# Performance work log

Hardware: AMD Instinct MI355X
Metric: run time of the kernel (lower is better)

Reference implementation:

```python
import jax, jax.numpy as jnp
import numpy as np
from jax import lax

N, L, D = 8, 2048, 512
KS = [3, 5]
DECAY = 0.2


def setup_inputs() -> dict:
    key = jax.random.key(0)
    k1, k2, k3, k4, k5 = jax.random.split(key, 5)
    return {
        "qa_embed_data": jax.random.normal(k1, (N, L, D), dtype=jnp.float32),
        "conv_w3": jax.random.normal(k2, (D, 1, KS[0]), dtype=jnp.float32) * (1.0 / KS[0]),
        "conv_w5": jax.random.normal(k3, (D, 1, KS[1]), dtype=jnp.float32) * (1.0 / KS[1]),
        "fusion_w": jax.random.normal(k4, (D, 2 * D), dtype=jnp.float32) * 0.02,
        "fusion_b": jax.random.normal(k5, (D,), dtype=jnp.float32) * 0.02,
    }


def causal_depthwise_conv(x, w, k):
    # x: [N, L, C], w: [C, 1, k] (depthwise, groups=C). Left-pad by k-1 (causal).
    xc = jnp.transpose(x, (0, 2, 1))  # [N, C, L]
    y = lax.conv_general_dilated(
        xc, w, window_strides=(1,), padding=[(k - 1, 0)],
        feature_group_count=x.shape[-1],
        dimension_numbers=("NCH", "OIH", "NCH"))
    return jnp.transpose(y, (0, 2, 1))  # [N, L, C]


def squash(v):
    norm = jnp.linalg.norm(v, axis=-1, keepdims=True)
    scale = norm ** 2 / (1.0 + norm ** 2)
    return scale * v / (norm + 1e-9)


def dynamic_routing(u, num_iterations):
    # u: [N, L, M, C]
    n, l, m, _ = u.shape
    logits = jnp.zeros((n, l, m), dtype=u.dtype)
    v = None
    for i in range(num_iterations):
        c = jax.nn.softmax(logits, axis=-1)
        s = jnp.einsum("nlm,nlmc->nlc", c, u)
        v = squash(s)
        if i < num_iterations - 1:
            logits = logits + jnp.einsum("nlmc,nlc->nlm", u, v)
    return v


def time_attention(x):
    # x: [N, L, C]; causal attention with exp(-decay*dist) bias -> add -decay*dist in log space
    l = x.shape[1]
    sim = jnp.einsum("nlc,nmc->nlm", x, x)  # [N, L, L]
    idx = jnp.arange(l)
    dist = (idx[:, None] - idx[None, :]).astype(x.dtype)  # query - key
    mask = dist >= 0  # lower-triangular causal mask
    ws = jnp.where(mask[None], sim - DECAY * dist[None], -jnp.inf)
    attn = jax.nn.softmax(ws, axis=-1)
    return jnp.einsum("nlm,nmc->nlc", attn, x)


def reference(qa_embed_data, conv_w3, conv_w5, fusion_w, fusion_b):
    trend3 = causal_depthwise_conv(qa_embed_data, conv_w3, KS[0])
    trend5 = causal_depthwise_conv(qa_embed_data, conv_w5, KS[1])
    seasonal = jnp.stack([qa_embed_data - trend3, qa_embed_data - trend5], axis=2)  # [N,L,2,C]
    trend = jnp.stack([trend3, trend5], axis=2)  # [N,L,2,C]
    seasonal_f = time_attention(dynamic_routing(seasonal, 3))
    trend_f = time_attention(dynamic_routing(trend, 3))
    cat = jnp.concatenate([seasonal_f, trend_f], axis=-1)  # [N,L,2C]
    return cat @ fusion_w.T + fusion_b
```

## Files before the change

kernel.cpp:

```cpp
#include <hip/hip_runtime.h>


typedef short     bf16x8 __attribute__((ext_vector_type(8)));
typedef float     f32x4  __attribute__((ext_vector_type(4)));
typedef unsigned short u16;
typedef u16       u16x8  __attribute__((ext_vector_type(8)));
typedef u16       u16x4  __attribute__((ext_vector_type(4)));

#define NBATCH 8
#define LSEQ   2048
#define DCH    512
#define DPAD   520
#define VSTR   40
#define DECAYF 0.2f
#define WTILES 4

typedef const __attribute__((address_space(1))) unsigned char* gas_t;
typedef __attribute__((address_space(3))) unsigned char* las_t;
__device__ __forceinline__ void dma16(const void* g, void* l) {
    __builtin_amdgcn_global_load_lds((gas_t)g, (las_t)l, 16, 0, 0);
}

__device__ __forceinline__ u16 f2bf(float f) {
    unsigned int u = __float_as_uint(f);
    u += 0x7fffu + ((u >> 16) & 1u);
    return (u16)(u >> 16);
}

__device__ __forceinline__ void wave_sum6(float& a, float& b, float& c,
                                          float& d, float& e, float& f) {
#pragma unroll
    for (int m = 1; m < 64; m <<= 1) {
        float ta = __shfl_xor(a, m, 64);
        float tb = __shfl_xor(b, m, 64);
        float tc = __shfl_xor(c, m, 64);
        float td = __shfl_xor(d, m, 64);
        float te = __shfl_xor(e, m, 64);
        float tf = __shfl_xor(f, m, 64);
        a += ta; b += tb; c += tc; d += td; e += te; f += tf;
    }
}

__global__ __launch_bounds__(256) void conv_route(
    const float* __restrict__ x, const float* __restrict__ w3, const float* __restrict__ w5,
    u16* __restrict__ vs, u16* __restrict__ vt)
{
    const int wid  = threadIdx.x >> 6;
    const int lane = threadIdx.x & 63;
    const int p = blockIdx.x * 4 + wid;
    const int n = p >> 11, l = p & (LSEQ - 1);
    const int c0 = lane * 8;

    float xm[5][8];
#pragma unroll
    for (int j = 0; j < 5; ++j) {
        int ll = l - j;
        if (ll >= 0) {
            const float4* sp = (const float4*)(x + ((size_t)(n*LSEQ + ll))*DCH + c0);
            float4 a = sp[0], b = sp[1];
            xm[j][0]=a.x; xm[j][1]=a.y; xm[j][2]=a.z; xm[j][3]=a.w;
            xm[j][4]=b.x; xm[j][5]=b.y; xm[j][6]=b.z; xm[j][7]=b.w;
        } else {
#pragma unroll
            for (int i = 0; i < 8; ++i) xm[j][i] = 0.f;
        }
    }
    float f3[24], f5[40];
#pragma unroll
    for (int k = 0; k < 6; ++k)  ((float4*)f3)[k] = ((const float4*)(w3 + (size_t)c0*3))[k];
#pragma unroll
    for (int k = 0; k < 10; ++k) ((float4*)f5)[k] = ((const float4*)(w5 + (size_t)c0*5))[k];

    float t3[8], t5[8], a0[8], a1[8];
#pragma unroll
    for (int i = 0; i < 8; ++i) {
        t3[i] = f3[i*3+0]*xm[2][i] + f3[i*3+1]*xm[1][i] + f3[i*3+2]*xm[0][i];
        t5[i] = f5[i*5+0]*xm[4][i] + f5[i*5+1]*xm[3][i] + f5[i*5+2]*xm[2][i]
              + f5[i*5+3]*xm[1][i] + f5[i*5+4]*xm[0][i];
        a0[i] = xm[0][i] - t3[i];
        a1[i] = xm[0][i] - t5[i];
    }

    float A1=0.f, B1=0.f, C1=0.f, A2=0.f, B2=0.f, C2=0.f;
#pragma unroll
    for (int i = 0; i < 8; ++i) {
        A1 += a0[i]*a0[i]; B1 += a0[i]*a1[i]; C1 += a1[i]*a1[i];
        A2 += t3[i]*t3[i]; B2 += t3[i]*t5[i]; C2 += t5[i]*t5[i];
    }
    wave_sum6(A1, B1, C1, A2, B2, C2);

    float ba0=0.f, ba1=0.f, bb0=0.f, bb1=0.f;
    float ca0=0.5f, ca1=0.5f, sca=0.f, cb0=0.5f, cb1=0.5f, scb=0.f;
#pragma unroll
    for (int it = 0; it < 3; ++it) {
        float mxa = fmaxf(ba0, ba1), mxb = fmaxf(bb0, bb1);
        float ea0 = __expf(ba0-mxa), ea1 = __expf(ba1-mxa);
        float eb0 = __expf(bb0-mxb), eb1 = __expf(bb1-mxb);
        float ia = 1.f/(ea0+ea1), ib = 1.f/(eb0+eb1);
        ca0 = ea0*ia; ca1 = ea1*ia; cb0 = eb0*ib; cb1 = eb1*ib;
        float na = ca0*ca0*A1 + 2.f*ca0*ca1*B1 + ca1*ca1*C1;
        float nb = cb0*cb0*A2 + 2.f*cb0*cb1*B2 + cb1*cb1*C2;
        sca = na / ((1.f + na) * (sqrtf(na) + 1e-9f));
        scb = nb / ((1.f + nb) * (sqrtf(nb) + 1e-9f));
        if (it < 2) {
            ba0 += sca*(ca0*A1 + ca1*B1);
            ba1 += sca*(ca0*B1 + ca1*C1);
            bb0 += scb*(cb0*A2 + cb1*B2);
            bb1 += scb*(cb0*B2 + cb1*C2);
        }
    }
    u16x8 pa, pb;
#pragma unroll
    for (int i = 0; i < 8; ++i) {
        pa[i] = f2bf(sca*(ca0*a0[i] + ca1*a1[i]));
        pb[i] = f2bf(scb*(cb0*t3[i] + cb1*t5[i]));
    }
    *(u16x8*)(vs + (size_t)p*DPAD + c0) = pa;
    *(u16x8*)(vt + (size_t)p*DPAD + c0) = pb;
}

__global__ __launch_bounds__(256) void attn(
    const u16* __restrict__ vs, const u16* __restrict__ vt,
    u16* __restrict__ cat)
{
    __shared__ u16 Ks[33792/2];
    __shared__ u16 Vs[DCH*VSTR];
    __shared__ unsigned int Ps32[4][16][20];

    const int inst = blockIdx.y;
    const int t = inst >> 3, n = inst & 7;
    const u16* src = (t ? vt : vs) + (size_t)n * LSEQ * DPAD;

    const int bx = blockIdx.x;
    const int r0 = (((bx & 7) << 2) | (bx >> 3)) * 64;

    const int tid  = threadIdx.x;
    const int wid  = tid >> 6, lane = tid & 63;
    const int l16  = lane & 15, quad = lane >> 4;

    bf16x8 qf[16];
    {
        const u16* qp = src + (size_t)(r0 + wid*16 + l16) * DPAD + quad*8;
#pragma unroll
        for (int kc = 0; kc < 16; ++kc) qf[kc] = *(const bf16x8*)(qp + kc*32);
    }

    f32x4 O[32];
#pragma unroll
    for (int i = 0; i < 32; ++i) O[i] = (f32x4){0.f, 0.f, 0.f, 0.f};
    f32x4 O2 = {0.f, 0.f, 0.f, 0.f};

    bf16x8 ones8;
#pragma unroll
    for (int i = 0; i < 8; ++i) ones8[i] = (short)0x3F80;

    const int kb_hi = (r0 >> 5) + 1;
    const int kb_lo = (kb_hi >= WTILES) ? kb_hi - (WTILES-1) : 0;

    {
        const u16* gK = src + (size_t)kb_lo * 32 * DPAD;
        for (int i = wid; i < 33; i += 4) dma16(gK + i*512 + lane*8, Ks + i*512);
    }

    for (int kb = kb_lo; kb <= kb_hi; ++kb) {
        __syncthreads();

        f32x4 S0a = {0.f,0.f,0.f,0.f}, S1a = {0.f,0.f,0.f,0.f};
        f32x4 S0b = {0.f,0.f,0.f,0.f}, S1b = {0.f,0.f,0.f,0.f};
#pragma unroll
        for (int kc = 0; kc < 8; ++kc) {
            bf16x8 b0 = *(const bf16x8*)(Ks + (size_t)l16*DPAD + kc*32 + quad*8);
            bf16x8 b1 = *(const bf16x8*)(Ks + (size_t)(16+l16)*DPAD + kc*32 + quad*8);
            S0a = __builtin_amdgcn_mfma_f32_16x16x32_bf16(qf[kc], b0, S0a, 0, 0, 0);
            S1a = __builtin_amdgcn_mfma_f32_16x16x32_bf16(qf[kc], b1, S1a, 0, 0, 0);
        }
#pragma unroll
        for (int kc = 8; kc < 16; ++kc) {
            bf16x8 b0 = *(const bf16x8*)(Ks + (size_t)l16*DPAD + kc*32 + quad*8);
            bf16x8 b1 = *(const bf16x8*)(Ks + (size_t)(16+l16)*DPAD + kc*32 + quad*8);
            S0b = __builtin_amdgcn_mfma_f32_16x16x32_bf16(qf[kc], b0, S0b, 0, 0, 0);
            S1b = __builtin_amdgcn_mfma_f32_16x16x32_bf16(qf[kc], b1, S1b, 0, 0, 0);
        }
        f32x4 S0 = S0a + S0b, S1 = S1a + S1b;

#pragma unroll
        for (int pass = 0; pass < 2; ++pass) {
            const int ch = pass*256 + tid;
#pragma unroll
            for (int g = 0; g < 4; ++g) {
                u16x8 o;
#pragma unroll
                for (int j = 0; j < 4; ++j) {
                    o[2*j]   = Ks[(size_t)(g*4 + j)      * DPAD + ch];
                    o[2*j+1] = Ks[(size_t)(g*4 + j + 16) * DPAD + ch];
                }
                *(u16x8*)(Vs + ch*VSTR + g*8) = o;
            }
        }

        const int rowg = r0 + wid*16 + quad*4;
#pragma unroll
        for (int r = 0; r < 4; ++r) {
            int row = rowg + r;
            int d0  = row - (kb*32 + l16);
            int d1  = d0 - 16;
            float p0 = (d0 >= 0) ? __expf(fmaf(-DECAYF, (float)d0, S0[r] - 1.f)) : 0.f;
            float p1 = (d1 >= 0) ? __expf(fmaf(-DECAYF, (float)d1, S1[r] - 1.f)) : 0.f;
            Ps32[wid][quad*4 + r][l16] = ((unsigned)f2bf(p1) << 16) | (unsigned)f2bf(p0);
        }

        __syncthreads();
        if (kb < kb_hi) {
            const u16* gK = src + (size_t)(kb+1) * 32 * DPAD;
            for (int i = wid; i < 33; i += 4) dma16(gK + i*512 + lane*8, Ks + i*512);
        }

        bf16x8 pf = *(const bf16x8*)(&Ps32[wid][l16][quad*4]);
#pragma unroll
        for (int ct = 0; ct < 32; ++ct) {
            bf16x8 vf = *(const bf16x8*)(Vs + (size_t)(ct*16 + l16)*VSTR + quad*8);
            O[ct] = __builtin_amdgcn_mfma_f32_16x16x32_bf16(pf, vf, O[ct], 0, 0, 0);
        }
        O2 = __builtin_amdgcn_mfma_f32_16x16x32_bf16(pf, ones8, O2, 0, 0, 0);
    }

    float inv[4];
#pragma unroll
    for (int r = 0; r < 4; ++r) inv[r] = 1.f / O2[r];
    const size_t rowbase = (size_t)n * LSEQ + r0 + wid*16 + quad*4;
    const int colbase = t * 512 + l16;
#pragma unroll
    for (int ct = 0; ct < 32; ++ct) {
#pragma unroll
        for (int r = 0; r < 4; ++r)
            cat[(rowbase + r) * 1024 + colbase + ct*16] = f2bf(O[ct][r] * inv[r]);
    }
}

__global__ __launch_bounds__(256) void cast_w(const float* __restrict__ w, u16* __restrict__ wb)
{
    int id = blockIdx.x * 256 + threadIdx.x;
    float4 f = ((const float4*)w)[id];
    u16x4 o;
    o[0] = f2bf(f.x); o[1] = f2bf(f.y); o[2] = f2bf(f.z); o[3] = f2bf(f.w);
    ((u16x4*)wb)[id] = o;
}

__global__ __launch_bounds__(256) void fusion_gemm(
    const u16* __restrict__ A, const u16* __restrict__ Wb,
    const float* __restrict__ bias, float* __restrict__ out)
{
    __shared__ u16 As[64*64];
    __shared__ u16 Bs[128*64];
    const int m0 = blockIdx.x * 64;
    const int n0 = blockIdx.y * 128;
    const int tid = threadIdx.x;
    const int wid = tid >> 6, lane = tid & 63;
    const int l16 = lane & 15, quad = lane >> 4;

    f32x4 acc[4][2];
#pragma unroll
    for (int i = 0; i < 4; ++i)
#pragma unroll
        for (int j = 0; j < 2; ++j) acc[i][j] = (f32x4){0.f, 0.f, 0.f, 0.f};

    for (int kb = 0; kb < 16; ++kb) {
        __syncthreads();
#pragma unroll
        for (int i = 0; i < 2; ++i) {
            int q = i*256 + tid, r = q >> 3, kp = q & 7;
            int kl = kp ^ (r & 7);
            dma16(A + (size_t)(m0 + r)*1024 + kb*64 + kl*8, As + q*8);
        }
#pragma unroll
        for (int i = 0; i < 4; ++i) {
            int q = i*256 + tid, r = q >> 3, kp = q & 7;
            int kl = kp ^ (r & 7);
            dma16(Wb + (size_t)(n0 + r)*1024 + kb*64 + kl*8, Bs + q*8);
        }
        __syncthreads();
#pragma unroll
        for (int k2 = 0; k2 < 2; ++k2) {
            const int kl = k2*4 + quad;
            bf16x8 af[4], bf2[2];
#pragma unroll
            for (int i = 0; i < 4; ++i) {
                int r = i*16 + l16;
                af[i] = *(const bf16x8*)(As + r*64 + (kl ^ (r & 7))*8);
            }
#pragma unroll
            for (int j = 0; j < 2; ++j) {
                int r = wid*32 + j*16 + l16;
                bf2[j] = *(const bf16x8*)(Bs + r*64 + (kl ^ (r & 7))*8);
            }
#pragma unroll
            for (int i = 0; i < 4; ++i)
#pragma unroll
                for (int j = 0; j < 2; ++j)
                    acc[i][j] = __builtin_amdgcn_mfma_f32_16x16x32_bf16(af[i], bf2[j], acc[i][j], 0, 0, 0);
        }
    }
#pragma unroll
    for (int j = 0; j < 2; ++j) {
        int col = n0 + wid*32 + j*16 + l16;
        float bv = bias[col];
#pragma unroll
        for (int i = 0; i < 4; ++i) {
            int rowb = m0 + i*16 + quad*4;
#pragma unroll
            for (int r = 0; r < 4; ++r)
                out[(size_t)(rowb + r)*512 + col] = acc[i][j][r] + bv;
        }
    }
}

extern "C" void kernel_launch(void* const* d_in, const int* in_sizes, int n_in,
                              void* d_out, int out_size, void* d_ws, size_t ws_size,
                              hipStream_t stream)
{
    (void)in_sizes; (void)n_in; (void)out_size; (void)ws_size;
    const float* x  = (const float*)d_in[0];
    const float* w3 = (const float*)d_in[1];
    const float* w5 = (const float*)d_in[2];
    const float* fw = (const float*)d_in[3];
    const float* fb = (const float*)d_in[4];
    float* out = (float*)d_out;

    const size_t SZP = (size_t)NBATCH * LSEQ * DPAD;
    u16* vs   = (u16*)d_ws;
    u16* vt   = vs   + SZP;
    u16* cat  = vt   + SZP;
    u16* wb   = cat  + (size_t)NBATCH*LSEQ*1024;

    cast_w     <<<512, 256, 0, stream>>>(fw, wb);
    conv_route <<<4096, 256, 0, stream>>>(x, w3, w5, vs, vt);
    attn       <<<dim3(32, 16), 256, 0, stream>>>(vs, vt, cat);
    fusion_gemm<<<dim3(256, 4), 256, 0, stream>>>(cat, wb, fb, out);
}
```

Before: 167.7 us.

## Double-buffer fusion GEMM LDS loads and split conv_route rows across two waves

The fusion GEMM now keeps two LDS buffers and issues the global-to-LDS DMA for the next K block before computing on the current one, so load latency overlaps MFMA work. conv_route now assigns each row to two waves of four channels per lane instead of one wave of eight, merging the partial dot products through shared memory and a block barrier, and launches twice as many blocks. This raises parallelism in conv_route at the cost of an extra barrier. The GEMM doubles its LDS use, which may lower occupancy.

```diff
diff --git a/kernel.cpp b/kernel.cpp
--- a/kernel.cpp
+++ b/kernel.cpp
@@ -47,33 +47,33 @@
 {
     const int wid  = threadIdx.x >> 6;
     const int lane = threadIdx.x & 63;
-    const int p = blockIdx.x * 4 + wid;
+    const int pp   = wid >> 1;
+    const int half = wid & 1;
+    const int p = blockIdx.x * 2 + pp;
     const int n = p >> 11, l = p & (LSEQ - 1);
-    const int c0 = lane * 8;
-
-    float xm[5][8];
+    const int c0 = half * 256 + lane * 4;
+
+    float xm[5][4];
 #pragma unroll
     for (int j = 0; j < 5; ++j) {
         int ll = l - j;
         if (ll >= 0) {
-            const float4* sp = (const float4*)(x + ((size_t)(n*LSEQ + ll))*DCH + c0);
-            float4 a = sp[0], b = sp[1];
+            float4 a = *(const float4*)(x + ((size_t)(n*LSEQ + ll))*DCH + c0);
             xm[j][0]=a.x; xm[j][1]=a.y; xm[j][2]=a.z; xm[j][3]=a.w;
-            xm[j][4]=b.x; xm[j][5]=b.y; xm[j][6]=b.z; xm[j][7]=b.w;
         } else {
 #pragma unroll
-            for (int i = 0; i < 8; ++i) xm[j][i] = 0.f;
-        }
-    }
-    float f3[24], f5[40];
-#pragma unroll
-    for (int k = 0; k < 6; ++k)  ((float4*)f3)[k] = ((const float4*)(w3 + (size_t)c0*3))[k];
-#pragma unroll
-    for (int k = 0; k < 10; ++k) ((float4*)f5)[k] = ((const float4*)(w5 + (size_t)c0*5))[k];
-
-    float t3[8], t5[8], a0[8], a1[8];
-#pragma unroll
-    for (int i = 0; i < 8; ++i) {
+            for (int i = 0; i < 4; ++i) xm[j][i] = 0.f;
+        }
+    }
+    float f3[12], f5[20];
+#pragma unroll
+    for (int k = 0; k < 3; ++k) ((float4*)f3)[k] = ((const float4*)(w3 + (size_t)c0*3))[k];
+#pragma unroll
+    for (int k = 0; k < 5; ++k) ((float4*)f5)[k] = ((const float4*)(w5 + (size_t)c0*5))[k];
+
+    float t3[4], t5[4], a0[4], a1[4];
+#pragma unroll
+    for (int i = 0; i < 4; ++i) {
         t3[i] = f3[i*3+0]*xm[2][i] + f3[i*3+1]*xm[1][i] + f3[i*3+2]*xm[0][i];
         t5[i] = f5[i*5+0]*xm[4][i] + f5[i*5+1]*xm[3][i] + f5[i*5+2]*xm[2][i]
               + f5[i*5+3]*xm[1][i] + f5[i*5+4]*xm[0][i];
@@ -83,11 +83,24 @@
 
     float A1=0.f, B1=0.f, C1=0.f, A2=0.f, B2=0.f, C2=0.f;
 #pragma unroll
-    for (int i = 0; i < 8; ++i) {
+    for (int i = 0; i < 4; ++i) {
         A1 += a0[i]*a0[i]; B1 += a0[i]*a1[i]; C1 += a1[i]*a1[i];
         A2 += t3[i]*t3[i]; B2 += t3[i]*t5[i]; C2 += t5[i]*t5[i];
     }
     wave_sum6(A1, B1, C1, A2, B2, C2);
+
+    __shared__ float red[2][2][6];
+    if (lane == 0) {
+        red[pp][half][0] = A1; red[pp][half][1] = B1; red[pp][half][2] = C1;
+        red[pp][half][3] = A2; red[pp][half][4] = B2; red[pp][half][5] = C2;
+    }
+    __syncthreads();
+    A1 = red[pp][0][0] + red[pp][1][0];
+    B1 = red[pp][0][1] + red[pp][1][1];
+    C1 = red[pp][0][2] + red[pp][1][2];
+    A2 = red[pp][0][3] + red[pp][1][3];
+    B2 = red[pp][0][4] + red[pp][1][4];
+    C2 = red[pp][0][5] + red[pp][1][5];
 
     float ba0=0.f, ba1=0.f, bb0=0.f, bb1=0.f;
     float ca0=0.5f, ca1=0.5f, sca=0.f, cb0=0.5f, cb1=0.5f, scb=0.f;
@@ -109,14 +122,14 @@
             bb1 += scb*(cb0*B2 + cb1*C2);
         }
     }
-    u16x8 pa, pb;
-#pragma unroll
-    for (int i = 0; i < 8; ++i) {
+    u16x4 pa, pb;
+#pragma unroll
+    for (int i = 0; i < 4; ++i) {
         pa[i] = f2bf(sca*(ca0*a0[i] + ca1*a1[i]));
         pb[i] = f2bf(scb*(cb0*t3[i] + cb1*t5[i]));
     }
-    *(u16x8*)(vs + (size_t)p*DPAD + c0) = pa;
-    *(u16x8*)(vt + (size_t)p*DPAD + c0) = pb;
+    *(u16x4*)(vs + (size_t)p*DPAD + c0) = pa;
+    *(u16x4*)(vt + (size_t)p*DPAD + c0) = pb;
 }
 
 __global__ __launch_bounds__(256) void attn(
@@ -250,8 +263,8 @@
     const u16* __restrict__ A, const u16* __restrict__ Wb,
     const float* __restrict__ bias, float* __restrict__ out)
 {
-    __shared__ u16 As[64*64];
-    __shared__ u16 Bs[128*64];
+    __shared__ u16 As[2][64*64];
+    __shared__ u16 Bs[2][128*64];
     const int m0 = blockIdx.x * 64;
     const int n0 = blockIdx.y * 128;
     const int tid = threadIdx.x;
@@ -264,21 +277,28 @@
 #pragma unroll
         for (int j = 0; j < 2; ++j) acc[i][j] = (f32x4){0.f, 0.f, 0.f, 0.f};
 
-    for (int kb = 0; kb < 16; ++kb) {
-        __syncthreads();
+    auto stage = [&](int kb_, int b_) {
 #pragma unroll
         for (int i = 0; i < 2; ++i) {
             int q = i*256 + tid, r = q >> 3, kp = q & 7;
             int kl = kp ^ (r & 7);
-            dma16(A + (size_t)(m0 + r)*1024 + kb*64 + kl*8, As + q*8);
+            dma16(A + (size_t)(m0 + r)*1024 + kb_*64 + kl*8, As[b_] + q*8);
         }
 #pragma unroll
         for (int i = 0; i < 4; ++i) {
             int q = i*256 + tid, r = q >> 3, kp = q & 7;
             int kl = kp ^ (r & 7);
-            dma16(Wb + (size_t)(n0 + r)*1024 + kb*64 + kl*8, Bs + q*8);
-        }
-        __syncthreads();
+            dma16(Wb + (size_t)(n0 + r)*1024 + kb_*64 + kl*8, Bs[b_] + q*8);
+        }
+    };
+
+    stage(0, 0);
+    for (int kb = 0; kb < 16; ++kb) {
+        const int b = kb & 1;
+        asm volatile("s_waitcnt vmcnt(0)" ::: "memory");
+        __builtin_amdgcn_s_barrier();
+        asm volatile("" ::: "memory");
+        if (kb < 15) stage(kb + 1, b ^ 1);
 #pragma unroll
         for (int k2 = 0; k2 < 2; ++k2) {
             const int kl = k2*4 + quad;
@@ -286,12 +306,12 @@
 #pragma unroll
             for (int i = 0; i < 4; ++i) {
                 int r = i*16 + l16;
-                af[i] = *(const bf16x8*)(As + r*64 + (kl ^ (r & 7))*8);
+                af[i] = *(const bf16x8*)(As[b] + r*64 + (kl ^ (r & 7))*8);
             }
 #pragma unroll
             for (int j = 0; j < 2; ++j) {
                 int r = wid*32 + j*16 + l16;
-                bf2[j] = *(const bf16x8*)(Bs + r*64 + (kl ^ (r & 7))*8);
+                bf2[j] = *(const bf16x8*)(Bs[b] + r*64 + (kl ^ (r & 7))*8);
             }
 #pragma unroll
             for (int i = 0; i < 4; ++i)
@@ -333,7 +353,7 @@
     u16* wb   = cat  + (size_t)NBATCH*LSEQ*1024;
 
     cast_w     <<<512, 256, 0, stream>>>(fw, wb);
-    conv_route <<<4096, 256, 0, stream>>>(x, w3, w5, vs, vt);
+    conv_route <<<8192, 256, 0, stream>>>(x, w3, w5, vs, vt);
     attn       <<<dim3(32, 16), 256, 0, stream>>>(vs, vt, cat);
     fusion_gemm<<<dim3(256, 4), 256, 0, stream>>>(cat, wb, fb, out);
 }
```

Measured after the change: 183.8 us. +9.6%, slower.
